# Optimization experiments

Measured on AMD Instinct MI355X. Metric: run time of the kernel, lower is better.

Reference implementation:

```python
import jax, jax.numpy as jnp
import numpy as np

BATCH = 2048
IN_DIM = 4096
OUT_DIM = 1024
N_EDGES = 16384  # mat_wann.connection_count
CONSTANT_WEIGHT = 1.0


def setup_inputs() -> dict:
    key = jax.random.key(0)
    k1, k2, k3 = jax.random.split(key, 3)
    x = jax.random.normal(k1, (BATCH, IN_DIM), dtype=jnp.float32)
    # one scalar Linear(1,1,bias=False) per connection, all init to constant_weight
    weights = jnp.ones((N_EDGES,), dtype=jnp.float32) * CONSTANT_WEIGHT
    # edge list: src input column, dst output node (sorted => segment-friendly)
    edge_src = jax.random.randint(k2, (N_EDGES,), 0, IN_DIM, dtype=jnp.int32)
    edge_dst = jnp.sort(jax.random.randint(k3, (N_EDGES,), 0, OUT_DIM, dtype=jnp.int32))
    return {"x": x, "weights": weights, "edge_src": edge_src, "edge_dst": edge_dst}


def reference(x, weights, edge_src, edge_dst):
    # gather per-edge input column and apply the per-edge scalar linear
    contrib = x[:, edge_src] * weights[None, :]              # [B, E]
    # scatter-add (segment-reduce) per-edge contributions into output nodes
    node_sums = jax.ops.segment_sum(contrib.T, edge_dst, num_segments=OUT_DIM)  # [OUT_DIM, B]
    # per-node activation (self.activations[...]); nodes with no incoming edges
    # stay zero, matching torch.zeros for empty rows since tanh(0)=0
    h = jnp.tanh(node_sums.T)                                 # [B, OUT_DIM]
    # activation_list applied to concatenated outputs
    return jax.nn.sigmoid(h)
```

## Files before the change

kernel.cpp:

```cpp
#include <hip/hip_runtime.h>
#include <math.h>

#define BATCH   2048
#define IN_DIM  4096
#define OUT_DIM 1024
#define N_EDGES 16384

#define R   2
#define NPT 4

__global__ __launch_bounds__(256) void prep_kernel(
        const int* __restrict__ edge_dst,
        const int* __restrict__ edge_src,
        const float* __restrict__ weights,
        int* __restrict__ node_off,
        int2* __restrict__ epack) {
    const int i = blockIdx.x * 256 + threadIdx.x;
    if (i < N_EDGES)
        epack[i] = make_int2(edge_src[i], __float_as_int(weights[i]));
    if (i <= OUT_DIM) {
        int lo = 0, hi = N_EDGES;
        while (lo < hi) {
            int mid = (lo + hi) >> 1;
            if (edge_dst[mid] < i) lo = mid + 1; else hi = mid;
        }
        node_off[i] = lo;
    }
}

__global__ __launch_bounds__(256) void fused_kernel(
        const float* __restrict__ x,
        const int2* __restrict__ epack,
        const int* __restrict__ node_off,
        float* __restrict__ out) {
    __shared__ float xs[R * IN_DIM];

    const int brow = blockIdx.x * R;

    const float4* src4 = (const float4*)(x + (size_t)brow * IN_DIM);
    float4* xs4 = (float4*)xs;
#pragma unroll
    for (int i = 0; i < (R * IN_DIM / 4) / 256; i++)
        xs4[threadIdx.x + i * 256] = src4[threadIdx.x + i * 256];
    __syncthreads();

    const int node0 = threadIdx.x * NPT;
    const int4 o4 = *(const int4*)(node_off + node0);
    const int oend = node_off[node0 + NPT];
    const int lo[NPT + 1] = {o4.x, o4.y, o4.z, o4.w, oend};

    float v0[NPT], v1[NPT];
#pragma unroll
    for (int n = 0; n < NPT; n++) {
        float a0 = 0.0f, a1 = 0.0f;
#pragma unroll 4
        for (int e = lo[n]; e < lo[n + 1]; e++) {
            const int2 p = epack[e];
            const float w = __int_as_float(p.y);
            a0 = fmaf(w, xs[p.x], a0);
            a1 = fmaf(w, xs[IN_DIM + p.x], a1);
        }
        const float h0 = tanhf(a0);
        const float h1 = tanhf(a1);
        v0[n] = 1.0f / (1.0f + expf(-h0));
        v1[n] = 1.0f / (1.0f + expf(-h1));
    }

    *(float4*)(out + (size_t)(brow + 0) * OUT_DIM + node0) =
        make_float4(v0[0], v0[1], v0[2], v0[3]);
    *(float4*)(out + (size_t)(brow + 1) * OUT_DIM + node0) =
        make_float4(v1[0], v1[1], v1[2], v1[3]);
}

extern "C" void kernel_launch(void* const* d_in, const int* in_sizes, int n_in,
                              void* d_out, int out_size, void* d_ws, size_t ws_size,
                              hipStream_t stream) {
    const float* x        = (const float*)d_in[0];
    const float* weights  = (const float*)d_in[1];
    const int*   edge_src = (const int*)d_in[2];
    const int*   edge_dst = (const int*)d_in[3];
    float*       out      = (float*)d_out;

    int*  node_off = (int*)d_ws;
    int2* epack    = (int2*)((char*)d_ws + 8192);

    prep_kernel<<<N_EDGES / 256, 256, 0, stream>>>(
        edge_dst, edge_src, weights, node_off, epack);

    fused_kernel<<<BATCH / R, 256, 0, stream>>>(x, epack, node_off, out);
}
```

Measured before the change: 101.9 us.

## Use padded ELL edge layout with one node per thread and 2D grid

```diff
diff --git a/kernel.cpp b/kernel.cpp
--- a/kernel.cpp
+++ b/kernel.cpp
@@ -6,70 +6,79 @@
 #define OUT_DIM 1024
 #define N_EDGES 16384
 
-#define R   2
-#define NPT 4
+#define R    4
+#define LCAP 64
 
 __global__ __launch_bounds__(256) void prep_kernel(
         const int* __restrict__ edge_dst,
         const int* __restrict__ edge_src,
         const float* __restrict__ weights,
-        int* __restrict__ node_off,
-        int2* __restrict__ epack) {
-    const int i = blockIdx.x * 256 + threadIdx.x;
-    if (i < N_EDGES)
-        epack[i] = make_int2(edge_src[i], __float_as_int(weights[i]));
-    if (i <= OUT_DIM) {
-        int lo = 0, hi = N_EDGES;
-        while (lo < hi) {
-            int mid = (lo + hi) >> 1;
-            if (edge_dst[mid] < i) lo = mid + 1; else hi = mid;
-        }
-        node_off[i] = lo;
+        int2* __restrict__ epack2,
+        int* __restrict__ lmaxw) {
+    const int n = blockIdx.x * 256 + threadIdx.x;
+    int lo = 0, hi = N_EDGES;
+    while (lo < hi) {
+        int mid = (lo + hi) >> 1;
+        if (edge_dst[mid] < n) lo = mid + 1; else hi = mid;
     }
+    int lo2 = lo, hi2 = N_EDGES;
+    while (lo2 < hi2) {
+        int mid = (lo2 + hi2) >> 1;
+        if (edge_dst[mid] < n + 1) lo2 = mid + 1; else hi2 = mid;
+    }
+    int deg = lo2 - lo;
+    if (deg > LCAP) deg = LCAP;
+
+    const int nb = n >> 8, t = n & 255;
+    int2* dst = epack2 + (size_t)nb * LCAP * 256 + t;
+    for (int i = 0; i < deg; i++) {
+        const int e = lo + i;
+        dst[i * 256] = make_int2(edge_src[e], __float_as_int(weights[e]));
+    }
+    atomicMax(&lmaxw[n >> 6], deg);
 }
 
-__global__ __launch_bounds__(256) void fused_kernel(
+__global__ __launch_bounds__(256, 2) void fused_kernel(
         const float* __restrict__ x,
-        const int2* __restrict__ epack,
-        const int* __restrict__ node_off,
+        const int2* __restrict__ epack2,
+        const int* __restrict__ lmaxw,
         float* __restrict__ out) {
     __shared__ float xs[R * IN_DIM];
 
-    const int brow = blockIdx.x * R;
+    const int nb = blockIdx.x;
+    const int brow = blockIdx.y * R;
+    const int t = threadIdx.x;
 
-    const float4* src4 = (const float4*)(x + (size_t)brow * IN_DIM);
-    float4* xs4 = (float4*)xs;
+    const float4* s4 = (const float4*)(x + (size_t)brow * IN_DIM);
+    float4* d4 = (float4*)xs;
 #pragma unroll
     for (int i = 0; i < (R * IN_DIM / 4) / 256; i++)
-        xs4[threadIdx.x + i * 256] = src4[threadIdx.x + i * 256];
+        d4[t + i * 256] = s4[t + i * 256];
+
+    const int lmax = lmaxw[nb * 4 + (t >> 6)];
+    const int2* ep = epack2 + (size_t)nb * LCAP * 256 + t;
+
     __syncthreads();
 
-    const int node0 = threadIdx.x * NPT;
-    const int4 o4 = *(const int4*)(node_off + node0);
-    const int oend = node_off[node0 + NPT];
-    const int lo[NPT + 1] = {o4.x, o4.y, o4.z, o4.w, oend};
-
-    float v0[NPT], v1[NPT];
-#pragma unroll
-    for (int n = 0; n < NPT; n++) {
-        float a0 = 0.0f, a1 = 0.0f;
+    float a0 = 0.0f, a1 = 0.0f, a2 = 0.0f, a3 = 0.0f;
 #pragma unroll 4
-        for (int e = lo[n]; e < lo[n + 1]; e++) {
-            const int2 p = epack[e];
-            const float w = __int_as_float(p.y);
-            a0 = fmaf(w, xs[p.x], a0);
-            a1 = fmaf(w, xs[IN_DIM + p.x], a1);
-        }
-        const float h0 = tanhf(a0);
-        const float h1 = tanhf(a1);
-        v0[n] = 1.0f / (1.0f + expf(-h0));
-        v1[n] = 1.0f / (1.0f + expf(-h1));
+    for (int i = 0; i < lmax; i++) {
+        const int2 p = ep[i * 256];
+        const int s = p.x;
+        const float w = __int_as_float(p.y);
+        a0 = fmaf(w, xs[s], a0);
+        a1 = fmaf(w, xs[IN_DIM + s], a1);
+        a2 = fmaf(w, xs[2 * IN_DIM + s], a2);
+        a3 = fmaf(w, xs[3 * IN_DIM + s], a3);
     }
 
-    *(float4*)(out + (size_t)(brow + 0) * OUT_DIM + node0) =
-        make_float4(v0[0], v0[1], v0[2], v0[3]);
-    *(float4*)(out + (size_t)(brow + 1) * OUT_DIM + node0) =
-        make_float4(v1[0], v1[1], v1[2], v1[3]);
+    const int node = nb * 256 + t;
+    float acc[R] = {a0, a1, a2, a3};
+#pragma unroll
+    for (int r = 0; r < R; r++) {
+        const float h = tanhf(acc[r]);
+        out[(size_t)(brow + r) * OUT_DIM + node] = 1.0f / (1.0f + expf(-h));
+    }
 }
 
 extern "C" void kernel_launch(void* const* d_in, const int* in_sizes, int n_in,
@@ -81,11 +90,15 @@
     const int*   edge_dst = (const int*)d_in[3];
     float*       out      = (float*)d_out;
 
-    int*  node_off = (int*)d_ws;
-    int2* epack    = (int2*)((char*)d_ws + 8192);
+    int2* epack2 = (int2*)d_ws;
+    int*  lmaxw  = (int*)((char*)d_ws + (size_t)4 * LCAP * 256 * sizeof(int2));
 
-    prep_kernel<<<N_EDGES / 256, 256, 0, stream>>>(
-        edge_dst, edge_src, weights, node_off, epack);
+    hipMemsetAsync(d_ws, 0, (size_t)4 * LCAP * 256 * sizeof(int2) + 16 * sizeof(int),
+                   stream);
 
-    fused_kernel<<<BATCH / R, 256, 0, stream>>>(x, epack, node_off, out);
+    prep_kernel<<<OUT_DIM / 256, 256, 0, stream>>>(
+        edge_dst, edge_src, weights, epack2, lmaxw);
+
+    dim3 grid(OUT_DIM / 256, BATCH / R);
+    fused_kernel<<<grid, 256, 0, stream>>>(x, epack2, lmaxw, out);
 }
```

Result: slower. 127.9 us (+25.5%).
